# Kernel optimization log

Measured on AMD Instinct MI355X. Metric: run time of the kernel, lower is better.

## Reference

```python
import jax, jax.numpy as jnp
import numpy as np

# hparams (match init_kwargs)
EXP_LOW_BOUND = -8.0          # clip scores-max to [low_bound, 0]
EXP_CLIP_AND_SUBTRACT = True  # subtract exp(low_bound) from clipped tensor before exp
EXP_LINEAR_GRADIENT = 0.0     # 0 -> use true exp on the clipped/shifted tensor
EXP_SUM_HIGH_BOUND = 1024.0   # clamp the softmax denominator
RECIP_LINEAR_GRADIENT = 0.0   # 0 -> exact reciprocal
RECIP_LOW_BOUND = 0.0

B, S, H, D = 4, 1024, 16, 64


def _approx_exp(x):
    # exponential() from the source
    if EXP_LOW_BOUND != 0:
        x = jnp.clip(x, EXP_LOW_BOUND, 0.0)
    if EXP_CLIP_AND_SUBTRACT:
        x = x - np.float32(np.exp(EXP_LOW_BOUND))
    if EXP_LINEAR_GRADIENT:
        return jnp.clip(x * np.float32(EXP_LINEAR_GRADIENT) + 1.0, 0.0, 1.0)
    return jnp.exp(x)


def _approx_recip(x):
    # reciprocal() from the source
    if RECIP_LINEAR_GRADIENT != 0:
        g = np.float32(RECIP_LINEAR_GRADIENT)
        return jnp.clip((1.0 + g) - g * x, RECIP_LOW_BOUND, 1.0)
    return 1.0 / x


def _custom_softmax(a):
    # softmax() with exp_hparams / reciprocal_hparams path, norm over last axis
    amax = jnp.max(a, axis=-1, keepdims=True)
    amax = jnp.where(jnp.isfinite(amax), amax, 0.0)
    asubmax = a - amax
    approx_exp = _approx_exp(asubmax)                       # [B,H,Sq,Sk]
    asumexp = jnp.sum(approx_exp, axis=-1, keepdims=True)   # [B,H,Sq,1]
    if EXP_SUM_HIGH_BOUND:
        sum_low_bound = 1.0
        if EXP_LOW_BOUND != 0 and EXP_CLIP_AND_SUBTRACT:
            sum_low_bound = 1.0 - float(np.exp(EXP_LOW_BOUND))
        asumexp = jnp.clip(asumexp, sum_low_bound, EXP_SUM_HIGH_BOUND)
    return approx_exp * _approx_recip(asumexp)


def setup_inputs() -> dict:
    key = jax.random.key(0)
    kq, kk, kv = jax.random.split(key, 3)
    return {
        "query": jax.random.normal(kq, (B, S, H, D), dtype=jnp.float32),
        "key": jax.random.normal(kk, (B, S, H, D), dtype=jnp.float32),
        "value": jax.random.normal(kv, (B, S, H, D), dtype=jnp.float32),
    }


def reference(query, key, value):
    depth = query.shape[-1]
    q = query * (1.0 / np.sqrt(depth)).astype(np.float32)
    # scores: [B, H, Sq, Sk]
    scores = jnp.einsum("bqhd,bkhd->bhqk", q, key)
    weights = _custom_softmax(scores).astype(query.dtype)
    # output: [B, Sq, H, D]
    return jnp.einsum("bhqk,bkhd->bqhd", weights, value)
```

## Files before the change

### kernel.cpp

```cpp
#include <hip/hip_runtime.h>

#define BB 4
#define SS 1024
#define HH 16
#define DD 64
#define KTL 128
#define NT 256

typedef short bf16x8 __attribute__((ext_vector_type(8)));
typedef float f32x4 __attribute__((ext_vector_type(4)));

#define KP 72
#define VP 136
#define PP 136

__device__ __forceinline__ unsigned pk2(float a, float b) {
    unsigned ua = __float_as_uint(a) + 0x8000u;
    unsigned ub = __float_as_uint(b) + 0x8000u;
    return (ub & 0xffff0000u) | (ua >> 16);
}
__device__ __forceinline__ unsigned short f2bf(float a) {
    return (unsigned short)((__float_as_uint(a) + 0x8000u) >> 16);
}
__device__ __forceinline__ f32x4 mfma16(bf16x8 a, bf16x8 b, f32x4 c) {
    return __builtin_amdgcn_mfma_f32_16x16x32_bf16(a, b, c, 0, 0, 0);
}

__global__ __launch_bounds__(NT, 2)
void attn_flash(const float* __restrict__ q, const float* __restrict__ k,
                const float* __restrict__ v, float* __restrict__ out) {
    __shared__ unsigned short sK[KTL * KP];
    __shared__ unsigned short sVt[DD * VP];
    __shared__ unsigned short sP[4 * 32 * PP];

    const int t = threadIdx.x, lane = t & 63, w = t >> 6;
    const int n16 = lane & 15, quad = lane >> 4;

    const int bx = blockIdx.x;
    const int bh = bx & 63, qt = bx >> 6;
    const int h = bh & 15, b = bh >> 4;
    const int qbase = qt * 128 + w * 32;

    const float LOG2E = 1.44269504f;

    bf16x8 qf[2][2];
    #pragma unroll
    for (int s = 0; s < 2; ++s)
      #pragma unroll
      for (int ks = 0; ks < 2; ++ks) {
        const float* p = q + (((size_t)(b * SS + qbase + s * 16 + n16) * HH + h) * DD)
                           + ks * 32 + quad * 8;
        float4 x = ((const float4*)p)[0];
        float4 y = ((const float4*)p)[1];
        bf16x8 f;
        f[0] = (short)f2bf(x.x * 0.125f); f[1] = (short)f2bf(x.y * 0.125f);
        f[2] = (short)f2bf(x.z * 0.125f); f[3] = (short)f2bf(x.w * 0.125f);
        f[4] = (short)f2bf(y.x * 0.125f); f[5] = (short)f2bf(y.y * 0.125f);
        f[6] = (short)f2bf(y.z * 0.125f); f[7] = (short)f2bf(y.w * 0.125f);
        qf[s][ks] = f;
      }

    const size_t bh_off = ((size_t)b * SS * HH + h) * DD;
    const float4* kbase4 = (const float4*)(k + bh_off);
    const float4* vbase4 = (const float4*)(v + bh_off);
    const f32x4 zero = {0.f, 0.f, 0.f, 0.f};

    float m[2]  = {-1e30f, -1e30f};
    float su[2] = {0.f, 0.f};
    f32x4 oacc[2][4];
    #pragma unroll
    for (int s = 0; s < 2; ++s)
      #pragma unroll
      for (int dt = 0; dt < 4; ++dt) oacc[s][dt] = zero;

    const int krow = t >> 1, khalf = t & 1;
    const int va = t >> 4, vc = t & 15;
    unsigned short* sPw = sP + w * 32 * PP;

    for (int kt0 = 0; kt0 < SS; kt0 += KTL) {
        {
            const float4* kp = kbase4 + (size_t)(kt0 + krow) * 256 + khalf * 8;
            float4 r[8];
            #pragma unroll
            for (int i = 0; i < 8; ++i) r[i] = kp[i];
            unsigned short* dst = &sK[krow * KP + khalf * 32];
            #pragma unroll
            for (int u = 0; u < 4; ++u) {
                uint4 val;
                val.x = pk2(r[2*u].x, r[2*u].y);
                val.y = pk2(r[2*u].z, r[2*u].w);
                val.z = pk2(r[2*u+1].x, r[2*u+1].y);
                val.w = pk2(r[2*u+1].z, r[2*u+1].w);
                *(uint4*)&dst[u * 8] = val;
            }
        }
        {
            const float4* vp = vbase4 + (size_t)(kt0 + va * 8) * 256 + vc;
            float4 r[8];
            #pragma unroll
            for (int i = 0; i < 8; ++i) r[i] = vp[i * 256];
            #pragma unroll
            for (int comp = 0; comp < 4; ++comp) {
                const float* f0 = (const float*)&r[0];
                uint4 val;
                val.x = pk2(f0[0*4+comp], f0[1*4+comp]);
                val.y = pk2(f0[2*4+comp], f0[3*4+comp]);
                val.z = pk2(f0[4*4+comp], f0[5*4+comp]);
                val.w = pk2(f0[6*4+comp], f0[7*4+comp]);
                *(uint4*)&sVt[(vc * 4 + comp) * VP + va * 8] = val;
            }
        }
        __syncthreads();

        f32x4 S[2][8];
        #pragma unroll
        for (int ct = 0; ct < 8; ++ct) {
            bf16x8 k0 = *(const bf16x8*)&sK[(ct * 16 + n16) * KP + quad * 8];
            bf16x8 k1 = *(const bf16x8*)&sK[(ct * 16 + n16) * KP + 32 + quad * 8];
            S[0][ct] = mfma16(k1, qf[0][1], mfma16(k0, qf[0][0], zero));
            S[1][ct] = mfma16(k1, qf[1][1], mfma16(k0, qf[1][0], zero));
        }

        #pragma unroll
        for (int s = 0; s < 2; ++s) {
            float tm = S[s][0][0];
            #pragma unroll
            for (int ct = 0; ct < 8; ++ct)
              #pragma unroll
              for (int r = 0; r < 4; ++r) tm = fmaxf(tm, S[s][ct][r]);
            tm = fmaxf(tm, __shfl_xor(tm, 16));
            tm = fmaxf(tm, __shfl_xor(tm, 32));
            float mnew = fmaxf(m[s], tm);
            float al = __builtin_amdgcn_exp2f((m[s] - mnew) * LOG2E);
            m[s] = mnew;
            su[s] *= al;
            #pragma unroll
            for (int r = 0; r < 4; ++r) {
                float alq = __shfl(al, quad * 4 + r);
                #pragma unroll
                for (int dt = 0; dt < 4; ++dt) oacc[s][dt][r] *= alq;
            }
        }

        #pragma unroll
        for (int ct = 0; ct < 8; ++ct)
          #pragma unroll
          for (int s = 0; s < 2; ++s) {
            float e0, e1, e2, e3;
            {
                float x0 = fmaxf(S[s][ct][0] - m[s], -8.0f);
                float x1 = fmaxf(S[s][ct][1] - m[s], -8.0f);
                float x2 = fmaxf(S[s][ct][2] - m[s], -8.0f);
                float x3 = fmaxf(S[s][ct][3] - m[s], -8.0f);
                e0 = __builtin_amdgcn_exp2f(x0 * LOG2E);
                e1 = __builtin_amdgcn_exp2f(x1 * LOG2E);
                e2 = __builtin_amdgcn_exp2f(x2 * LOG2E);
                e3 = __builtin_amdgcn_exp2f(x3 * LOG2E);
            }
            su[s] += (e0 + e1) + (e2 + e3);
            *(uint2*)&sPw[(s * 16 + n16) * PP + ct * 16 + quad * 4] =
                make_uint2(pk2(e0, e1), pk2(e2, e3));
          }

        #pragma unroll
        for (int ks = 0; ks < 4; ++ks) {
            bf16x8 pf0 = *(const bf16x8*)&sPw[n16 * PP + ks * 32 + quad * 8];
            bf16x8 pf1 = *(const bf16x8*)&sPw[(16 + n16) * PP + ks * 32 + quad * 8];
            #pragma unroll
            for (int dt = 0; dt < 4; ++dt) {
                bf16x8 vf = *(const bf16x8*)&sVt[(dt * 16 + n16) * VP + ks * 32 + quad * 8];
                oacc[0][dt] = mfma16(pf0, vf, oacc[0][dt]);
                oacc[1][dt] = mfma16(pf1, vf, oacc[1][dt]);
            }
        }
        __syncthreads();
    }

    #pragma unroll
    for (int s = 0; s < 2; ++s) {
        su[s] += __shfl_xor(su[s], 16);
        su[s] += __shfl_xor(su[s], 32);
    }
    const float F  = 0.99966460f;
    const float LO = 0.99966454f;
    #pragma unroll
    for (int s = 0; s < 2; ++s) {
        float denom = fminf(fmaxf(su[s] * F, LO), 1024.0f);
        float sc = F / denom;
        #pragma unroll
        for (int r = 0; r < 4; ++r) {
            float scq = __shfl(sc, quad * 4 + r);
            #pragma unroll
            for (int dt = 0; dt < 4; ++dt) {
                size_t off = ((size_t)(b * SS + qbase + s * 16 + quad * 4 + r) * HH + h) * DD
                           + dt * 16 + n16;
                out[off] = oacc[s][dt][r] * scq;
            }
        }
    }
}

extern "C" void kernel_launch(void* const* d_in, const int* in_sizes, int n_in,
                              void* d_out, int out_size, void* d_ws, size_t ws_size,
                              hipStream_t stream) {
    const float* q = (const float*)d_in[0];
    const float* k = (const float*)d_in[1];
    const float* v = (const float*)d_in[2];
    float* o = (float*)d_out;
    dim3 grid(BB * HH * (SS / 128));
    dim3 block(NT);
    hipLaunchKernelGGL(attn_flash, grid, block, 0, stream, q, k, v, o);
}
```

Before: 129.5 us.

## Keep P in registers via permuted K rows and transposed PV MFMA

Loads K rows in a permuted order so the exponentiated score fragments map directly onto the B-operand layout of the PV MFMA. This removes the shared-memory staging of P, and a lane shuffle supplies the missing halves. The PV product is computed transposed (V as A operand), so the per-row rescale and final normalization no longer need per-lane shuffles, and the output is written as float4. The block shrinks to 128 threads and 64 queries, which doubles the grid. K/V tiles are now loaded and converted twice as often per query, and V uses an XOR-swizzled layout.

```diff
diff --git a/kernel.cpp b/kernel.cpp
--- a/kernel.cpp
+++ b/kernel.cpp
@@ -5,14 +5,13 @@
 #define HH 16
 #define DD 64
 #define KTL 128
-#define NT 256
+#define NT 128
+#define QBLK 64
 
 typedef short bf16x8 __attribute__((ext_vector_type(8)));
 typedef float f32x4 __attribute__((ext_vector_type(4)));
 
 #define KP 72
-#define VP 136
-#define PP 136
 
 __device__ __forceinline__ unsigned pk2(float a, float b) {
     unsigned ua = __float_as_uint(a) + 0x8000u;
@@ -25,13 +24,16 @@
 __device__ __forceinline__ f32x4 mfma16(bf16x8 a, bf16x8 b, f32x4 c) {
     return __builtin_amdgcn_mfma_f32_16x16x32_bf16(a, b, c, 0, 0, 0);
 }
+__device__ __forceinline__ int sigma_row(int r) {
+    int a = (r >> 4) & 1, qs = (r >> 2) & 3, b = r & 3;
+    return (r & ~31) | ((qs ^ (b >> 1)) << 3) | (a << 2) | b;
+}
 
 __global__ __launch_bounds__(NT, 2)
-void attn_flash(const float* __restrict__ q, const float* __restrict__ k,
-                const float* __restrict__ v, float* __restrict__ out) {
+void attn_flash2(const float* __restrict__ q, const float* __restrict__ k,
+                 const float* __restrict__ v, float* __restrict__ out) {
     __shared__ unsigned short sK[KTL * KP];
-    __shared__ unsigned short sVt[DD * VP];
-    __shared__ unsigned short sP[4 * 32 * PP];
+    __shared__ unsigned short sVt[DD * KTL];
 
     const int t = threadIdx.x, lane = t & 63, w = t >> 6;
     const int n16 = lane & 15, quad = lane >> 4;
@@ -39,7 +41,7 @@
     const int bx = blockIdx.x;
     const int bh = bx & 63, qt = bx >> 6;
     const int h = bh & 15, b = bh >> 4;
-    const int qbase = qt * 128 + w * 32;
+    const int qbase = qt * QBLK + w * 32;
 
     const float LOG2E = 1.44269504f;
 
@@ -73,17 +75,19 @@
       #pragma unroll
       for (int dt = 0; dt < 4; ++dt) oacc[s][dt] = zero;
 
-    const int krow = t >> 1, khalf = t & 1;
-    const int va = t >> 4, vc = t & 15;
-    unsigned short* sPw = sP + w * 32 * PP;
+    const int khalf = t & 1, krow2 = t >> 1;
+    const int voct = t >> 4, vc = t & 15;
 
     for (int kt0 = 0; kt0 < SS; kt0 += KTL) {
-        {
-            const float4* kp = kbase4 + (size_t)(kt0 + krow) * 256 + khalf * 8;
+        #pragma unroll
+        for (int p = 0; p < 2; ++p) {
+            int row = p * 64 + krow2;
+            int gk = sigma_row(row);
+            const float4* kp = kbase4 + (size_t)(kt0 + gk) * 256 + khalf * 8;
             float4 r[8];
             #pragma unroll
             for (int i = 0; i < 8; ++i) r[i] = kp[i];
-            unsigned short* dst = &sK[krow * KP + khalf * 32];
+            unsigned short* dst = &sK[row * KP + khalf * 32];
             #pragma unroll
             for (int u = 0; u < 4; ++u) {
                 uint4 val;
@@ -94,20 +98,24 @@
                 *(uint4*)&dst[u * 8] = val;
             }
         }
-        {
-            const float4* vp = vbase4 + (size_t)(kt0 + va * 8) * 256 + vc;
+        #pragma unroll
+        for (int p = 0; p < 2; ++p) {
+            int o = voct + 8 * p;
+            const float4* vp = vbase4 + (size_t)(kt0 + o * 8) * 256 + vc;
             float4 r[8];
             #pragma unroll
             for (int i = 0; i < 8; ++i) r[i] = vp[i * 256];
-            #pragma unroll
-            for (int comp = 0; comp < 4; ++comp) {
-                const float* f0 = (const float*)&r[0];
+            const float* fr = (const float*)r;
+            #pragma unroll
+            for (int c = 0; c < 4; ++c) {
+                int d = 4 * vc + c;
+                int atomp = o ^ (vc & 7) ^ ((c & 1) << 2);
                 uint4 val;
-                val.x = pk2(f0[0*4+comp], f0[1*4+comp]);
-                val.y = pk2(f0[2*4+comp], f0[3*4+comp]);
-                val.z = pk2(f0[4*4+comp], f0[5*4+comp]);
-                val.w = pk2(f0[6*4+comp], f0[7*4+comp]);
-                *(uint4*)&sVt[(vc * 4 + comp) * VP + va * 8] = val;
+                val.x = pk2(fr[0*4+c], fr[1*4+c]);
+                val.y = pk2(fr[2*4+c], fr[3*4+c]);
+                val.z = pk2(fr[4*4+c], fr[5*4+c]);
+                val.w = pk2(fr[6*4+c], fr[7*4+c]);
+                *(uint4*)&sVt[d * 128 + atomp * 8] = val;
             }
         }
         __syncthreads();
@@ -115,8 +123,9 @@
         f32x4 S[2][8];
         #pragma unroll
         for (int ct = 0; ct < 8; ++ct) {
-            bf16x8 k0 = *(const bf16x8*)&sK[(ct * 16 + n16) * KP + quad * 8];
-            bf16x8 k1 = *(const bf16x8*)&sK[(ct * 16 + n16) * KP + 32 + quad * 8];
+            int base = (ct * 16 + n16) * KP + quad * 8;
+            bf16x8 k0 = *(const bf16x8*)&sK[base];
+            bf16x8 k1 = *(const bf16x8*)&sK[base + 32];
             S[0][ct] = mfma16(k1, qf[0][1], mfma16(k0, qf[0][0], zero));
             S[1][ct] = mfma16(k1, qf[1][1], mfma16(k0, qf[1][0], zero));
         }
@@ -135,44 +144,44 @@
             m[s] = mnew;
             su[s] *= al;
             #pragma unroll
-            for (int r = 0; r < 4; ++r) {
-                float alq = __shfl(al, quad * 4 + r);
-                #pragma unroll
-                for (int dt = 0; dt < 4; ++dt) oacc[s][dt][r] *= alq;
+            for (int dt = 0; dt < 4; ++dt) oacc[s][dt] *= al;
+        }
+
+        unsigned P0[2][8], P1[2][8];
+        #pragma unroll
+        for (int s = 0; s < 2; ++s)
+          #pragma unroll
+          for (int ct = 0; ct < 8; ++ct) {
+            float x0 = fmaxf(S[s][ct][0] - m[s], -8.0f);
+            float x1 = fmaxf(S[s][ct][1] - m[s], -8.0f);
+            float x2 = fmaxf(S[s][ct][2] - m[s], -8.0f);
+            float x3 = fmaxf(S[s][ct][3] - m[s], -8.0f);
+            float e0 = __builtin_amdgcn_exp2f(x0 * LOG2E);
+            float e1 = __builtin_amdgcn_exp2f(x1 * LOG2E);
+            float e2 = __builtin_amdgcn_exp2f(x2 * LOG2E);
+            float e3 = __builtin_amdgcn_exp2f(x3 * LOG2E);
+            su[s] += (e0 + e1) + (e2 + e3);
+            P0[s][ct] = pk2(e0, e1);
+            P1[s][ct] = pk2(e2, e3);
+          }
+
+        #pragma unroll
+        for (int s = 0; s < 2; ++s)
+          #pragma unroll
+          for (int ks = 0; ks < 4; ++ks) {
+            union { uint4 u; bf16x8 f; } pf;
+            pf.u.x = P0[s][2*ks];
+            pf.u.y = (unsigned)__shfl_xor((int)P1[s][2*ks], 16);
+            pf.u.z = P0[s][2*ks+1];
+            pf.u.w = (unsigned)__shfl_xor((int)P1[s][2*ks+1], 16);
+            #pragma unroll
+            for (int dt = 0; dt < 4; ++dt) {
+                int d = dt * 16 + n16;
+                int atomp = (4 * ks + quad) ^ ((d >> 2) & 7) ^ ((d & 1) << 2);
+                bf16x8 vf = *(const bf16x8*)&sVt[d * 128 + atomp * 8];
+                oacc[s][dt] = mfma16(vf, pf.f, oacc[s][dt]);
             }
-        }
-
-        #pragma unroll
-        for (int ct = 0; ct < 8; ++ct)
-          #pragma unroll
-          for (int s = 0; s < 2; ++s) {
-            float e0, e1, e2, e3;
-            {
-                float x0 = fmaxf(S[s][ct][0] - m[s], -8.0f);
-                float x1 = fmaxf(S[s][ct][1] - m[s], -8.0f);
-                float x2 = fmaxf(S[s][ct][2] - m[s], -8.0f);
-                float x3 = fmaxf(S[s][ct][3] - m[s], -8.0f);
-                e0 = __builtin_amdgcn_exp2f(x0 * LOG2E);
-                e1 = __builtin_amdgcn_exp2f(x1 * LOG2E);
-                e2 = __builtin_amdgcn_exp2f(x2 * LOG2E);
-                e3 = __builtin_amdgcn_exp2f(x3 * LOG2E);
-            }
-            su[s] += (e0 + e1) + (e2 + e3);
-            *(uint2*)&sPw[(s * 16 + n16) * PP + ct * 16 + quad * 4] =
-                make_uint2(pk2(e0, e1), pk2(e2, e3));
           }
-
-        #pragma unroll
-        for (int ks = 0; ks < 4; ++ks) {
-            bf16x8 pf0 = *(const bf16x8*)&sPw[n16 * PP + ks * 32 + quad * 8];
-            bf16x8 pf1 = *(const bf16x8*)&sPw[(16 + n16) * PP + ks * 32 + quad * 8];
-            #pragma unroll
-            for (int dt = 0; dt < 4; ++dt) {
-                bf16x8 vf = *(const bf16x8*)&sVt[(dt * 16 + n16) * VP + ks * 32 + quad * 8];
-                oacc[0][dt] = mfma16(pf0, vf, oacc[0][dt]);
-                oacc[1][dt] = mfma16(pf1, vf, oacc[1][dt]);
-            }
-        }
         __syncthreads();
     }
 
@@ -188,14 +197,15 @@
         float denom = fminf(fmaxf(su[s] * F, LO), 1024.0f);
         float sc = F / denom;
         #pragma unroll
-        for (int r = 0; r < 4; ++r) {
-            float scq = __shfl(sc, quad * 4 + r);
-            #pragma unroll
-            for (int dt = 0; dt < 4; ++dt) {
-                size_t off = ((size_t)(b * SS + qbase + s * 16 + quad * 4 + r) * HH + h) * DD
-                           + dt * 16 + n16;
-                out[off] = oacc[s][dt][r] * scq;
-            }
+        for (int dt = 0; dt < 4; ++dt) {
+            float4 val;
+            val.x = oacc[s][dt][0] * sc;
+            val.y = oacc[s][dt][1] * sc;
+            val.z = oacc[s][dt][2] * sc;
+            val.w = oacc[s][dt][3] * sc;
+            size_t off = ((size_t)(b * SS + qbase + s * 16 + n16) * HH + h) * DD
+                       + dt * 16 + quad * 4;
+            *(float4*)&out[off] = val;
         }
     }
 }
@@ -207,7 +217,7 @@
     const float* k = (const float*)d_in[1];
     const float* v = (const float*)d_in[2];
     float* o = (float*)d_out;
-    dim3 grid(BB * HH * (SS / 128));
+    dim3 grid(BB * HH * (SS / QBLK));
     dim3 block(NT);
-    hipLaunchKernelGGL(attn_flash, grid, block, 0, stream, q, k, v, o);
-}
+    hipLaunchKernelGGL(attn_flash2, grid, block, 0, stream, q, k, v, o);
+}
```

New measurement: 139.6 us. 7.8% more time.
